# Optimization experiments

Hardware: AMD Instinct MI355X
Metric: run time of the kernel (lower is better)

The kernel has to match this reference:

```python
import jax, jax.numpy as jnp
import numpy as np

N = 100000   # points
L = 4        # SAM mask features per point (MHA kv length)
D = 256      # embed dim (out_pt_fea_dim == MHA embed_dim)
H = 4        # heads
GY = 200     # voxel grid extent used for xy_ind
C = 16       # fea_compre

def _bn(x, g, b, m, v):
    # eval-mode BatchNorm1d
    return (x - m) * jax.lax.rsqrt(v + 1e-5) * g + b

def setup_inputs():
    key = jax.random.key(0)
    ks = jax.random.split(key, 48)
    f32 = jnp.float32
    rn = lambda i, sh, s=0.05: jax.random.normal(ks[i], sh, dtype=f32) * s
    ru = lambda i, sh: jax.random.uniform(ks[i], sh, dtype=f32) + 0.5
    inp = {}
    inp['pt_fea'] = jax.random.normal(ks[0], (N, 3), dtype=f32)
    inp['xy_ind'] = jax.random.randint(ks[1], (N, 2), 0, GY, dtype=jnp.int32)
    inp['segfea'] = jax.random.normal(ks[2], (N, L, D), dtype=f32)
    inp['pixfea'] = jax.random.normal(ks[3], (N, D), dtype=f32)
    # PPmodel params (weights stored [in,out])
    dims = [3, 64, 128, 256]
    for j, d in enumerate(dims):
        inp[f'bn{j}_g'] = ru(4 + j, (d,))
        inp[f'bn{j}_b'] = rn(8 + j, (d,))
        inp[f'bn{j}_m'] = rn(12 + j, (d,))
        inp[f'bn{j}_v'] = ru(16 + j, (d,))
    inp['W1'], inp['b1'] = rn(20, (3, 64), 0.3), rn(21, (64,))
    inp['W2'], inp['b2'] = rn(22, (64, 128), 0.1), rn(23, (128,))
    inp['W3'], inp['b3'] = rn(24, (128, 256), 0.08), rn(25, (256,))
    inp['W4'], inp['b4'] = rn(26, (256, D), 0.06), rn(27, (D,))
    # MultiheadAttention params
    inp['Wq'], inp['bq'] = rn(28, (D, D)), rn(29, (D,))
    inp['Wk'], inp['bk'] = rn(30, (D, D)), rn(31, (D,))
    inp['Wv'], inp['bv'] = rn(32, (D, D)), rn(33, (D,))
    inp['Wo'], inp['bo'] = rn(34, (D, D)), rn(35, (D,))
    # to_128 and fea_compression
    inp['W128'], inp['b128'] = rn(36, (D, 128), 0.06), rn(37, (128,))
    inp['Wc'], inp['bc'] = rn(38, (128, C), 0.1), rn(39, (C,))
    return inp

def reference(pt_fea, xy_ind, segfea, pixfea,
              bn0_g, bn0_b, bn0_m, bn0_v, W1, b1,
              bn1_g, bn1_b, bn1_m, bn1_v, W2, b2,
              bn2_g, bn2_b, bn2_m, bn2_v, W3, b3,
              bn3_g, bn3_b, bn3_m, bn3_v, W4, b4,
              Wq, bq, Wk, bk, Wv, bv, Wo, bo,
              W128, b128, Wc, bc):
    # PPmodel: BN -> (Lin,BN,ReLU) x3 -> Lin
    x = _bn(pt_fea, bn0_g, bn0_b, bn0_m, bn0_v)
    x = jax.nn.relu(_bn(x @ W1 + b1, bn1_g, bn1_b, bn1_m, bn1_v))
    x = jax.nn.relu(_bn(x @ W2 + b2, bn2_g, bn2_b, bn2_m, bn2_v))
    x = jax.nn.relu(_bn(x @ W3 + b3, bn3_g, bn3_b, bn3_m, bn3_v))
    mlp = x @ W4 + b4                                   # [N, D]
    # MultiheadAttention (batch_first, query len 1, eval -> no dropout)
    dh = D // H
    q = (mlp @ Wq + bq).reshape(N, H, dh)               # [N,H,dh]
    k = (segfea @ Wk + bk).reshape(N, L, H, dh)
    v = (segfea @ Wv + bv).reshape(N, L, H, dh)
    scores = jnp.einsum('nhd,nlhd->nhl', q, k) / jnp.sqrt(jnp.float32(dh))
    attn = jax.nn.softmax(scores, axis=-1)              # [N,H,L]
    sam = jnp.einsum('nhl,nlhd->nhd', attn, v).reshape(N, D) @ Wo + bo  # [N,D]
    # unique voxel ids (single batch element -> pad index 0)
    keys = xy_ind[:, 0].astype(jnp.int32) * GY + xy_ind[:, 1].astype(jnp.int32)
    unq_keys, unq_inv, unq_cnt = jnp.unique(
        keys, return_inverse=True, return_counts=True, size=N, fill_value=GY * GY)
    valid = (unq_cnt > 0)[:, None]
    pool = lambda d: jnp.where(valid, jax.ops.segment_max(d, unq_inv, num_segments=N), 0.0)
    ori = pool(mlp) @ W128 + b128                       # scatter_max -> to_128
    seg_pooled = pool(sam)
    pix_pooled = pool(pixfea)
    processed = jax.nn.relu(ori @ Wc + bc)              # fea_compression
    unq = jnp.stack([jnp.zeros_like(unq_keys), unq_keys // GY, unq_keys % GY], axis=1).astype(jnp.int64)
    return (unq, processed, seg_pooled, pix_pooled, unq_inv)
```

## Files before the change

kernel.cpp:

```cpp
#include <hip/hip_runtime.h>
#include <math.h>
#include <stdint.h>

#define NPTS 100000
#define LKV 4
#define GYV 200
#define NBINS 40000

typedef __attribute__((ext_vector_type(8))) short bf16x8;
typedef __attribute__((ext_vector_type(8))) unsigned short u16x8;
typedef __attribute__((ext_vector_type(4))) float f32x4;

__device__ __forceinline__ unsigned short bfr(float f) {
    unsigned u = __float_as_uint(f);
    unsigned r = (u + 0x7fffu + ((u >> 16) & 1u)) >> 16;
    return (unsigned short)r;
}
__device__ __forceinline__ float fbf(unsigned short h) {
    return __uint_as_float(((unsigned)h) << 16);
}

__device__ __forceinline__ unsigned fenc(float f) {
    unsigned u = __float_as_uint(f);
    return (u & 0x80000000u) ? ~u : (u | 0x80000000u);
}
__device__ __forceinline__ float fdec(unsigned u) {
    unsigned b = (u & 0x80000000u) ? (u & 0x7fffffffu) : ~u;
    return __uint_as_float(b);
}

__global__ void kZ(unsigned* __restrict__ seg_u, unsigned* __restrict__ pix_u,
                   int* __restrict__ count)
{
    size_t idx = (size_t)blockIdx.x * 256 + threadIdx.x;
    const size_t SEG = (size_t)NPTS * 256;
    if (idx < SEG)            seg_u[idx] = 0u;
    else if (idx < 2 * SEG)   pix_u[idx - SEG] = 0u;
    else if (idx < 2 * SEG + NBINS) count[idx - 2 * SEG] = 0;
}

__global__ void kH(const int* __restrict__ xy, int* __restrict__ keys,
                   int* __restrict__ count)
{
    int i = blockIdx.x * 256 + threadIdx.x;
    if (i < NPTS) {
        int key = xy[i * 2] * GYV + xy[i * 2 + 1];
        keys[i] = key;
        atomicAdd(count + key, 1);
    }
}

__global__ __launch_bounds__(1024) void kScan(
    const int* __restrict__ count, int* __restrict__ rank,
    int* __restrict__ unqk, int* __restrict__ total)
{
    __shared__ int swcnt[16];
    __shared__ int carry_s;
    const int t = threadIdx.x, lane = t & 63, wid = t >> 6;
    if (t == 0) carry_s = 0;
    for (int chunk = 0; chunk < 40; ++chunk) {
        __syncthreads();
        int idx = chunk * 1024 + t;
        int pres = (idx < NBINS && count[idx] > 0) ? 1 : 0;
        unsigned long long mask = __ballot(pres);
        int lanepre = __popcll(mask & ((1ull << lane) - 1ull));
        if (lane == 0) swcnt[wid] = __popcll(mask);
        __syncthreads();
        if (t == 0) {
            int s = carry_s;
            for (int w = 0; w < 16; ++w) { int cn = swcnt[w]; swcnt[w] = s; s += cn; }
            carry_s = s;
        }
        __syncthreads();
        if (pres) { int e = swcnt[wid] + lanepre; rank[idx] = e; unqk[e] = idx; }
    }
    __syncthreads();
    if (t == 0) total[0] = carry_s;
}

__global__ void kU(const int* __restrict__ unqk, const int* __restrict__ total,
                   float* __restrict__ out_unq)
{
    int j = blockIdx.x * 256 + threadIdx.x;
    if (j < NPTS) {
        int k = (j < total[0]) ? unqk[j] : NBINS;
        out_unq[j * 3 + 0] = 0.f;
        out_unq[j * 3 + 1] = (float)(k / GYV);
        out_unq[j * 3 + 2] = (float)(k % GYV);
    }
}

__global__ void kConvW(const float* __restrict__ W, unsigned short* __restrict__ dst,
                       int KD, int OD)
{
    int gid = blockIdx.x * 256 + threadIdx.x;
    if (gid >= KD * OD) return;
    int k = gid / OD, n = gid - k * OD;
    int idx = ((((k >> 5) * (OD >> 4) + (n >> 4)) * 4 + ((k >> 3) & 3)) * 16 + (n & 15)) * 8 + (k & 7);
    dst[idx] = bfr(W[gid]);
}

__global__ void kConvW2(const float* __restrict__ W, unsigned short* __restrict__ dh,
                        unsigned short* __restrict__ dl, int KD, int OD)
{
    int gid = blockIdx.x * 256 + threadIdx.x;
    if (gid >= KD * OD) return;
    int k = gid / OD, n = gid - k * OD;
    int idx = ((((k >> 5) * (OD >> 4) + (n >> 4)) * 4 + ((k >> 3) & 3)) * 16 + (n & 15)) * 8 + (k & 7);
    float x = W[gid];
    unsigned short h = bfr(x);
    dh[idx] = h;
    dl[idx] = bfr(x - fbf(h));
}

template <int KD, int NTILES_TOT, int NT>
__device__ __forceinline__ void mfma_acc(
    const unsigned short* __restrict__ inbuf, const unsigned short* __restrict__ wf,
    int w, int quad, int c16, f32x4 (&acc)[4][NT])
{
    constexpr int KT = KD / 32;
    const f32x4 zz = {0.f, 0.f, 0.f, 0.f};
#pragma unroll
    for (int mt = 0; mt < 4; ++mt)
#pragma unroll
        for (int nt = 0; nt < NT; ++nt) acc[mt][nt] = zz;
#pragma unroll
    for (int kt = 0; kt < KT; ++kt) {
        bf16x8 a[4], b[NT];
        const unsigned short* ap = inbuf + ((kt * 64 + c16) * 4 + quad) * 8;
#pragma unroll
        for (int mt = 0; mt < 4; ++mt) a[mt] = *reinterpret_cast<const bf16x8*>(ap + mt * 512);
#pragma unroll
        for (int nt = 0; nt < NT; ++nt) {
            const unsigned short* bp = wf +
                (size_t)(((kt * NTILES_TOT + w * NT + nt) * 4 + quad) * 16 + c16) * 8;
            b[nt] = *reinterpret_cast<const bf16x8*>(bp);
        }
#pragma unroll
        for (int mt = 0; mt < 4; ++mt)
#pragma unroll
            for (int nt = 0; nt < NT; ++nt)
                acc[mt][nt] = __builtin_amdgcn_mfma_f32_16x16x32_bf16(a[mt], b[nt], acc[mt][nt], 0, 0, 0);
    }
}

template <int NT>
__device__ __forceinline__ void epi_bn(
    f32x4 (&acc)[4][NT], const float* lb, const float* g, const float* bb,
    const float* m, const float* v, unsigned short* __restrict__ outbuf,
    int w, int quad, int c16)
{
#pragma unroll
    for (int nt = 0; nt < NT; ++nt) {
        int n = (w * NT + nt) * 16 + c16;
        float sc = g[n] * rsqrtf(v[n] + 1e-5f);
        float mb = m[n], bbv = bb[n], lbv = lb[n];
        int nbase = ((n >> 5) * 64) * 32 + ((n >> 3) & 3) * 8 + (n & 7);
#pragma unroll
        for (int mt = 0; mt < 4; ++mt)
#pragma unroll
            for (int r = 0; r < 4; ++r) {
                int row = mt * 16 + quad * 4 + r;
                float y = fmaxf((acc[mt][nt][r] + lbv - mb) * sc + bbv, 0.f);
                outbuf[nbase + row * 32] = bfr(y);
            }
    }
}

__global__ __launch_bounds__(256) void kA(
    const float* __restrict__ pt_fea,
    const int* __restrict__ keys, const int* __restrict__ rank,
    const float* g0, const float* b0, const float* m0, const float* v0,
    const float* W1, const float* b1, const float* g1, const float* bb1, const float* m1, const float* v1,
    const unsigned short* __restrict__ w2f, const float* b2, const float* g2, const float* bb2, const float* m2, const float* v2,
    const unsigned short* __restrict__ w3f, const float* b3, const float* g3, const float* bb3, const float* m3, const float* v3,
    const unsigned short* __restrict__ w4f, const float* b4,
    const unsigned short* __restrict__ wqf, const float* bq,
    unsigned short* __restrict__ q_out, unsigned* __restrict__ seg_u)
{
    __shared__ __attribute__((aligned(16))) unsigned short bufX[64 * 256];
    __shared__ __attribute__((aligned(16))) unsigned short bufY[64 * 256];
    __shared__ float ptl[64 * 3];
    __shared__ int invs[64];
    const int t = threadIdx.x, w = t >> 6, lane = t & 63;
    const int quad = lane >> 4, c16 = lane & 15;
    const int base = blockIdx.x * 64;

    if (t < 192) {
        int p = t / 3, c = t - p * 3;
        int gp = base + p; if (gp >= NPTS) gp = NPTS - 1;
        float x = pt_fea[gp * 3 + c];
        float s = g0[c] * rsqrtf(v0[c] + 1e-5f);
        ptl[t] = (x - m0[c]) * s + b0[c];
    }
    if (t < 64 && base + t < NPTS) invs[t] = rank[keys[base + t]];
    __syncthreads();

    {
        int p = t >> 2, o0 = (t & 3) * 16;
        float x0 = ptl[p * 3], x1 = ptl[p * 3 + 1], x2 = ptl[p * 3 + 2];
#pragma unroll
        for (int j = 0; j < 16; ++j) {
            int o = o0 + j;
            float y = x0 * W1[o] + x1 * W1[64 + o] + x2 * W1[128 + o] + b1[o];
            float s = g1[o] * rsqrtf(v1[o] + 1e-5f);
            y = fmaxf((y - m1[o]) * s + bb1[o], 0.f);
            int idx = ((o >> 5) * 64 + p) * 32 + ((o >> 3) & 3) * 8 + (o & 7);
            bufX[idx] = bfr(y);
        }
    }
    __syncthreads();

    {
        f32x4 acc[4][2];
        mfma_acc<64, 8, 2>(bufX, w2f, w, quad, c16, acc);
        epi_bn<2>(acc, b2, g2, bb2, m2, v2, bufY, w, quad, c16);
    }
    __syncthreads();

    {
        f32x4 acc[4][4];
        mfma_acc<128, 16, 4>(bufY, w3f, w, quad, c16, acc);
        epi_bn<4>(acc, b3, g3, bb3, m3, v3, bufX, w, quad, c16);
    }
    __syncthreads();

    {
        f32x4 acc[4][4];
        mfma_acc<256, 16, 4>(bufX, w4f, w, quad, c16, acc);
#pragma unroll
        for (int nt = 0; nt < 4; ++nt) {
            int n = (w * 4 + nt) * 16 + c16;
            float lbv = b4[n];
            int nbase = ((n >> 5) * 64) * 32 + ((n >> 3) & 3) * 8 + (n & 7);
#pragma unroll
            for (int mt = 0; mt < 4; ++mt)
#pragma unroll
                for (int r = 0; r < 4; ++r) {
                    int row = mt * 16 + quad * 4 + r;
                    float y = acc[mt][nt][r] + lbv;
                    bufY[nbase + row * 32] = bfr(y);
                    if (base + row < NPTS)
                        atomicMax(seg_u + (size_t)invs[row] * 256 + n, fenc(y));
                }
        }
    }
    __syncthreads();

    {
        f32x4 acc[4][4];
        mfma_acc<256, 16, 4>(bufY, wqf, w, quad, c16, acc);
#pragma unroll
        for (int nt = 0; nt < 4; ++nt) {
            int n = (w * 4 + nt) * 16 + c16;
            float lbv = bq[n];
#pragma unroll
            for (int mt = 0; mt < 4; ++mt)
#pragma unroll
                for (int r = 0; r < 4; ++r) {
                    int row = mt * 16 + quad * 4 + r;
                    if (base + row < NPTS)
                        q_out[(size_t)(base + row) * 256 + n] = bfr(acc[mt][nt][r] + lbv);
                }
        }
    }
}

__global__ __launch_bounds__(256) void kC1(
    unsigned* __restrict__ seg_u, const int* __restrict__ total,
    const unsigned short* __restrict__ w128h, const unsigned short* __restrict__ w128l,
    const float* __restrict__ b128,
    const float* __restrict__ Wc, const float* __restrict__ bc,
    float* __restrict__ out_proc)
{
    __shared__ __attribute__((aligned(16))) unsigned short sb[2 * 64 * 256];
    const int t = threadIdx.x, w = t >> 6, lane = t & 63;
    const int quad = lane >> 4, c16 = lane & 15;
    const int j0 = blockIdx.x * 64;
    const int tot = total[0];

    if (j0 >= tot) {
        const int c = t & 15, r0 = (t >> 4) * 4;
        float a = bc[c];
#pragma unroll 8
        for (int k = 0; k < 128; ++k) a += b128[k] * Wc[k * 16 + c];
        a = fmaxf(a, 0.f);
#pragma unroll
        for (int rr = 0; rr < 4; ++rr) {
            int j = j0 + r0 + rr;
            if (j < NPTS) out_proc[(size_t)j * 16 + c] = a;
        }
        return;
    }

    unsigned short* fragH = sb;
    unsigned short* fragL = sb + 64 * 256;

#pragma unroll
    for (int it = 0; it < 8; ++it) {
        int ch = it * 256 + t;
        int r = ch >> 5, k0 = (ch & 31) * 8;
        int j = j0 + r;
        float x[8];
        if (j < tot) {
            unsigned* src = seg_u + (size_t)j * 256 + k0;
            uint4 u0 = *reinterpret_cast<const uint4*>(src);
            uint4 u1 = *reinterpret_cast<const uint4*>(src + 4);
            x[0] = fdec(u0.x); x[1] = fdec(u0.y); x[2] = fdec(u0.z); x[3] = fdec(u0.w);
            x[4] = fdec(u1.x); x[5] = fdec(u1.y); x[6] = fdec(u1.z); x[7] = fdec(u1.w);
            uint4 z = {0u, 0u, 0u, 0u};
            *reinterpret_cast<uint4*>(src) = z;
            *reinterpret_cast<uint4*>(src + 4) = z;
        } else {
#pragma unroll
            for (int q = 0; q < 8; ++q) x[q] = 0.f;
        }
        u16x8 hv, lv;
#pragma unroll
        for (int q = 0; q < 8; ++q) {
            unsigned short h = bfr(x[q]);
            hv[q] = h;
            lv[q] = bfr(x[q] - fbf(h));
        }
        int idx = ((k0 >> 5) * 64 + r) * 32 + ((k0 >> 3) & 3) * 8;
        *reinterpret_cast<u16x8*>(fragH + idx) = hv;
        *reinterpret_cast<u16x8*>(fragL + idx) = lv;
    }
    __syncthreads();

    f32x4 acc[4][2];
    const f32x4 zz = {0.f, 0.f, 0.f, 0.f};
#pragma unroll
    for (int mt = 0; mt < 4; ++mt)
#pragma unroll
        for (int nt = 0; nt < 2; ++nt) acc[mt][nt] = zz;
#pragma unroll
    for (int kt = 0; kt < 8; ++kt) {
        const unsigned short* aph = fragH + ((kt * 64 + c16) * 4 + quad) * 8;
        const unsigned short* apl = fragL + ((kt * 64 + c16) * 4 + quad) * 8;
        bf16x8 ah[4], al[4];
#pragma unroll
        for (int mt = 0; mt < 4; ++mt) {
            ah[mt] = *reinterpret_cast<const bf16x8*>(aph + mt * 512);
            al[mt] = *reinterpret_cast<const bf16x8*>(apl + mt * 512);
        }
#pragma unroll
        for (int nt = 0; nt < 2; ++nt) {
            size_t boff = (size_t)(((kt * 8 + w * 2 + nt) * 4 + quad) * 16 + c16) * 8;
            bf16x8 bh = *reinterpret_cast<const bf16x8*>(w128h + boff);
            bf16x8 bl = *reinterpret_cast<const bf16x8*>(w128l + boff);
#pragma unroll
            for (int mt = 0; mt < 4; ++mt) {
                acc[mt][nt] = __builtin_amdgcn_mfma_f32_16x16x32_bf16(ah[mt], bh, acc[mt][nt], 0, 0, 0);
                acc[mt][nt] = __builtin_amdgcn_mfma_f32_16x16x32_bf16(al[mt], bh, acc[mt][nt], 0, 0, 0);
                acc[mt][nt] = __builtin_amdgcn_mfma_f32_16x16x32_bf16(ah[mt], bl, acc[mt][nt], 0, 0, 0);
            }
        }
    }
    __syncthreads();

    float* ori = reinterpret_cast<float*>(sb);
#pragma unroll
    for (int nt = 0; nt < 2; ++nt) {
        int n = (w * 2 + nt) * 16 + c16;
        float bv = b128[n];
#pragma unroll
        for (int mt = 0; mt < 4; ++mt)
#pragma unroll
            for (int r = 0; r < 4; ++r)
                ori[(mt * 16 + quad * 4 + r) * 132 + n] = acc[mt][nt][r] + bv;
    }
    __syncthreads();

    {
        const int c = t & 15, r0 = (t >> 4) * 4;
        float a0 = bc[c], a1 = a0, a2 = a0, a3 = a0;
#pragma unroll 8
        for (int k = 0; k < 128; ++k) {
            float wv = Wc[k * 16 + c];
            a0 += ori[(r0 + 0) * 132 + k] * wv;
            a1 += ori[(r0 + 1) * 132 + k] * wv;
            a2 += ori[(r0 + 2) * 132 + k] * wv;
            a3 += ori[(r0 + 3) * 132 + k] * wv;
        }
        float* dst = out_proc + (size_t)(j0 + r0) * 16 + c;
        dst[0]  = fmaxf(a0, 0.f);
        dst[16] = fmaxf(a1, 0.f);
        dst[32] = fmaxf(a2, 0.f);
        dst[48] = fmaxf(a3, 0.f);
    }
}

__global__ void kP(const float* __restrict__ pixfea,
                   const int* __restrict__ keys, const int* __restrict__ rank,
                   unsigned* __restrict__ pix_u, float* __restrict__ out_inv)
{
    size_t idx = (size_t)blockIdx.x * 256 + threadIdx.x;
    int i = (int)(idx >> 8), c = (int)(idx & 255);
    int inv = rank[keys[i]];
    atomicMax(pix_u + (size_t)inv * 256 + c, fenc(pixfea[idx]));
    if (c == 0) out_inv[i] = (float)inv;
}

__global__ __launch_bounds__(256) void kB(
    const float* __restrict__ segfea, const unsigned short* __restrict__ q_in,
    const int* __restrict__ keys, const int* __restrict__ rank,
    const unsigned short* __restrict__ wkf, const unsigned short* __restrict__ wvf,
    const unsigned short* __restrict__ wof,
    const float* __restrict__ bk, const float* __restrict__ bv,
    const float* __restrict__ bo,
    unsigned* __restrict__ seg_u)
{
    __shared__ __attribute__((aligned(16))) unsigned short x_lds[64 * 256];
    __shared__ __attribute__((aligned(16))) unsigned short av_lds[16 * 256];
    __shared__ int invs[16];
    const int t = threadIdx.x, w = t >> 6, lane = t & 63;
    const int quad = lane >> 4, c16 = lane & 15;
    const int base = blockIdx.x * 16;

    {
        const float4* gsrc = reinterpret_cast<const float4*>(segfea + (size_t)base * 4 * 256);
#pragma unroll
        for (int it = 0; it < 16; ++it) {
            int e4 = it * 256 + t;
            float4 v4 = gsrc[e4];
            int r = e4 >> 6;
            int k0 = (e4 & 63) * 4;
            int idx = (((k0 >> 5) * 64 + r) * 4 + ((k0 >> 3) & 3)) * 8 + (k0 & 7);
            ushort4 u4;
            u4.x = bfr(v4.x); u4.y = bfr(v4.y); u4.z = bfr(v4.z); u4.w = bfr(v4.w);
            *reinterpret_cast<ushort4*>(x_lds + idx) = u4;
        }
    }
    if (t < 16) invs[t] = rank[keys[base + t]];
    __syncthreads();

    f32x4 acc[4][4];
    const f32x4 zz = {0.f, 0.f, 0.f, 0.f};

    mfma_acc<256, 16, 4>(x_lds, wkf, w, quad, c16, acc);

    float bkv[4], qv[4][4];
#pragma unroll
    for (int nt = 0; nt < 4; ++nt) bkv[nt] = bk[w * 64 + nt * 16 + c16];
#pragma unroll
    for (int mt = 0; mt < 4; ++mt)
#pragma unroll
        for (int nt = 0; nt < 4; ++nt)
            qv[mt][nt] = fbf(q_in[(size_t)(base + mt * 4 + quad) * 256 + w * 64 + nt * 16 + c16]);

    float sc[4][4];
#pragma unroll
    for (int mt = 0; mt < 4; ++mt) {
#pragma unroll
        for (int r = 0; r < 4; ++r) sc[mt][r] = 0.f;
#pragma unroll
        for (int nt = 0; nt < 4; ++nt)
#pragma unroll
            for (int r = 0; r < 4; ++r)
                sc[mt][r] += (acc[mt][nt][r] + bkv[nt]) * qv[mt][nt];
    }
#pragma unroll
    for (int off = 1; off < 16; off <<= 1)
#pragma unroll
        for (int mt = 0; mt < 4; ++mt)
#pragma unroll
            for (int r = 0; r < 4; ++r) sc[mt][r] += __shfl_xor(sc[mt][r], off);

    float aw[4][4];
#pragma unroll
    for (int mt = 0; mt < 4; ++mt) {
        float mx = -INFINITY;
#pragma unroll
        for (int r = 0; r < 4; ++r) { sc[mt][r] *= 0.125f; mx = fmaxf(mx, sc[mt][r]); }
        float s = 0.f;
#pragma unroll
        for (int r = 0; r < 4; ++r) { float e = __expf(sc[mt][r] - mx); aw[mt][r] = e; s += e; }
        float inv = 1.f / s;
#pragma unroll
        for (int r = 0; r < 4; ++r) aw[mt][r] *= inv;
    }

    mfma_acc<256, 16, 4>(x_lds, wvf, w, quad, c16, acc);

    float bvv[4];
#pragma unroll
    for (int nt = 0; nt < 4; ++nt) bvv[nt] = bv[w * 64 + nt * 16 + c16];
#pragma unroll
    for (int mt = 0; mt < 4; ++mt) {
#pragma unroll
        for (int nt = 0; nt < 4; ++nt) {
            float o = bvv[nt];
#pragma unroll
            for (int r = 0; r < 4; ++r) o += aw[mt][r] * acc[mt][nt][r];
            int p = mt * 4 + quad;
            int d = w * 64 + nt * 16 + c16;
            int idx = (((d >> 5) * 16 + p) * 4 + ((d >> 3) & 3)) * 8 + (d & 7);
            av_lds[idx] = bfr(o);
        }
    }
    __syncthreads();

    f32x4 acc3[4];
#pragma unroll
    for (int nt = 0; nt < 4; ++nt) acc3[nt] = zz;
#pragma unroll
    for (int kt = 0; kt < 8; ++kt) {
        bf16x8 a = *reinterpret_cast<const bf16x8*>(av_lds + ((kt * 16 + c16) * 4 + quad) * 8);
        const unsigned short* bp = wof + (size_t)(((kt * 16 + w * 4) * 4 + quad) * 16 + c16) * 8;
#pragma unroll
        for (int nt = 0; nt < 4; ++nt) {
            bf16x8 b = *reinterpret_cast<const bf16x8*>(bp + nt * 512);
            acc3[nt] = __builtin_amdgcn_mfma_f32_16x16x32_bf16(a, b, acc3[nt], 0, 0, 0);
        }
    }
#pragma unroll
    for (int nt = 0; nt < 4; ++nt) {
        float bov = bo[w * 64 + nt * 16 + c16];
#pragma unroll
        for (int r = 0; r < 4; ++r) {
            int p = quad * 4 + r;
            float sam = acc3[nt][r] + bov;
            atomicMax(seg_u + (size_t)invs[p] * 256 + w * 64 + nt * 16 + c16, fenc(sam));
        }
    }
}

__global__ void kC2(unsigned* __restrict__ seg_u, unsigned* __restrict__ pix_u,
                    const int* __restrict__ total)
{
    size_t idx = (size_t)blockIdx.x * 256 + threadIdx.x;
    const size_t SEG = (size_t)NPTS * 256;
    int tot = total[0];
    unsigned* buf = (idx < SEG) ? seg_u : pix_u;
    size_t k = (idx < SEG) ? idx : (idx - SEG);
    int j = (int)(k >> 8);
    if (j < tot) buf[k] = __float_as_uint(fdec(buf[k]));
}

extern "C" void kernel_launch(void* const* d_in, const int* in_sizes, int n_in,
                              void* d_out, int out_size, void* d_ws, size_t ws_size,
                              hipStream_t stream)
{
    const float* pt_fea = (const float*)d_in[0];
    const int*   xy     = (const int*)d_in[1];
    const float* segfea = (const float*)d_in[2];
    const float* pixfea = (const float*)d_in[3];
    const float* g0 = (const float*)d_in[4],  *b0 = (const float*)d_in[5];
    const float* m0 = (const float*)d_in[6],  *v0 = (const float*)d_in[7];
    const float* g1 = (const float*)d_in[8],  *bb1 = (const float*)d_in[9];
    const float* m1 = (const float*)d_in[10], *v1 = (const float*)d_in[11];
    const float* g2 = (const float*)d_in[12], *bb2 = (const float*)d_in[13];
    const float* m2 = (const float*)d_in[14], *v2 = (const float*)d_in[15];
    const float* g3 = (const float*)d_in[16], *bb3 = (const float*)d_in[17];
    const float* m3 = (const float*)d_in[18], *v3 = (const float*)d_in[19];
    const float* W1 = (const float*)d_in[20], *b1 = (const float*)d_in[21];
    const float* W2 = (const float*)d_in[22], *b2 = (const float*)d_in[23];
    const float* W3 = (const float*)d_in[24], *b3 = (const float*)d_in[25];
    const float* W4 = (const float*)d_in[26], *b4 = (const float*)d_in[27];
    const float* Wq = (const float*)d_in[28], *bq = (const float*)d_in[29];
    const float* Wk = (const float*)d_in[30], *bk = (const float*)d_in[31];
    const float* Wv = (const float*)d_in[32], *bv = (const float*)d_in[33];
    const float* Wo = (const float*)d_in[34], *bo = (const float*)d_in[35];
    const float* W128 = (const float*)d_in[36], *b128 = (const float*)d_in[37];
    const float* Wc = (const float*)d_in[38], *bc = (const float*)d_in[39];

    float* out = (float*)d_out;
    float* out_unq  = out;
    float* out_proc = out + (size_t)NPTS * 3;
    unsigned* seg_u = (unsigned*)(out + (size_t)NPTS * 19);
    unsigned* pix_u = (unsigned*)(out + (size_t)NPTS * 275);
    float* out_inv  = out + (size_t)NPTS * 531;

    char* ws = (char*)d_ws;
    unsigned short* wf = (unsigned short*)ws;
    unsigned short* wkf = wf;
    unsigned short* wvf = wf + 65536;
    unsigned short* wof = wf + 131072;
    unsigned short* wqf = wf + 196608;
    unsigned short* w4f = wf + 262144;
    unsigned short* w3f = wf + 327680;
    unsigned short* w2f = wf + 360448;
    unsigned short* q_bf = wf + 368640;
    int* keys  = (int*)(ws + (size_t)368640 * 2 + (size_t)NPTS * 256 * 2);
    int* rank  = keys + NPTS;
    int* count = rank + NBINS;
    int* unqk  = count + NBINS;
    int* total = unqk + NPTS;
    uintptr_t p128 = ((uintptr_t)(total + 1) + 255u) & ~(uintptr_t)255u;
    unsigned short* w128h = (unsigned short*)p128;
    unsigned short* w128l = w128h + 32768;

    const int NB16 = NPTS / 16;
    const int NB64 = (NPTS + 63) / 64;
    const size_t ZTOT = 2 * (size_t)NPTS * 256 + NBINS;
    kZ<<<(int)((ZTOT + 255) / 256), 256, 0, stream>>>(seg_u, pix_u, count);
    kH<<<(NPTS + 255) / 256, 256, 0, stream>>>(xy, keys, count);
    kScan<<<1, 1024, 0, stream>>>(count, rank, unqk, total);
    kU<<<(NPTS + 255) / 256, 256, 0, stream>>>(unqk, total, out_unq);
    kConvW<<<256, 256, 0, stream>>>(Wk, wkf, 256, 256);
    kConvW<<<256, 256, 0, stream>>>(Wv, wvf, 256, 256);
    kConvW<<<256, 256, 0, stream>>>(Wo, wof, 256, 256);
    kConvW<<<256, 256, 0, stream>>>(Wq, wqf, 256, 256);
    kConvW<<<256, 256, 0, stream>>>(W4, w4f, 256, 256);
    kConvW<<<128, 256, 0, stream>>>(W3, w3f, 128, 256);
    kConvW<<<32, 256, 0, stream>>>(W2, w2f, 64, 128);
    kConvW2<<<128, 256, 0, stream>>>(W128, w128h, w128l, 256, 128);
    kA<<<NB64, 256, 0, stream>>>(pt_fea, keys, rank,
        g0, b0, m0, v0,
        W1, b1, g1, bb1, m1, v1,
        w2f, b2, g2, bb2, m2, v2,
        w3f, b3, g3, bb3, m3, v3,
        w4f, b4, wqf, bq, q_bf, seg_u);
    kC1<<<NB64, 256, 0, stream>>>(seg_u, total, w128h, w128l, b128, Wc, bc, out_proc);
    kP<<<NPTS, 256, 0, stream>>>(pixfea, keys, rank, pix_u, out_inv);
    kB<<<NB16, 256, 0, stream>>>(segfea, q_bf, keys, rank,
        wkf, wvf, wof, bk, bv, bo, seg_u);
    kC2<<<2 * NPTS, 256, 0, stream>>>(seg_u, pix_u, total);
}
```

Measured before the change: 1.325 ms.

## Shrink LDS in kA/kB, vectorize zero and decode kernels, prefetch q

kA halves bufY and reuses bufX for the W4 output, with an extra barrier before overwriting. kB aliases av_lds onto x_lds and hoists the q loads and inverse-index lookup ahead of the segfea staging. Both kernels gain launch_bounds occupancy hints. kZ and kC2 switch to uint4 vectorized accesses, cutting thread count fourfold. The aim is more resident blocks per CU and fewer memory transactions, at the cost of extra barriers and possible register pressure from the min-blocks hint.

```diff
diff --git a/kernel.cpp b/kernel.cpp
--- a/kernel.cpp
+++ b/kernel.cpp
@@ -29,14 +29,15 @@
     return __uint_as_float(b);
 }
 
-__global__ void kZ(unsigned* __restrict__ seg_u, unsigned* __restrict__ pix_u,
-                   int* __restrict__ count)
+__global__ void kZ(uint4* __restrict__ seg_u4, uint4* __restrict__ pix_u4,
+                   uint4* __restrict__ count4)
 {
     size_t idx = (size_t)blockIdx.x * 256 + threadIdx.x;
-    const size_t SEG = (size_t)NPTS * 256;
-    if (idx < SEG)            seg_u[idx] = 0u;
-    else if (idx < 2 * SEG)   pix_u[idx - SEG] = 0u;
-    else if (idx < 2 * SEG + NBINS) count[idx - 2 * SEG] = 0;
+    const size_t SEG4 = (size_t)NPTS * 64;
+    const uint4 z = {0u, 0u, 0u, 0u};
+    if (idx < SEG4)            seg_u4[idx] = z;
+    else if (idx < 2 * SEG4)   pix_u4[idx - SEG4] = z;
+    else if (idx < 2 * SEG4 + NBINS / 4) count4[idx - 2 * SEG4] = z;
 }
 
 __global__ void kH(const int* __restrict__ xy, int* __restrict__ keys,
@@ -167,7 +168,7 @@
     }
 }
 
-__global__ __launch_bounds__(256) void kA(
+__global__ __launch_bounds__(256, 4) void kA(
     const float* __restrict__ pt_fea,
     const int* __restrict__ keys, const int* __restrict__ rank,
     const float* g0, const float* b0, const float* m0, const float* v0,
@@ -179,7 +180,7 @@
     unsigned short* __restrict__ q_out, unsigned* __restrict__ seg_u)
 {
     __shared__ __attribute__((aligned(16))) unsigned short bufX[64 * 256];
-    __shared__ __attribute__((aligned(16))) unsigned short bufY[64 * 256];
+    __shared__ __attribute__((aligned(16))) unsigned short bufY[64 * 128];
     __shared__ float ptl[64 * 3];
     __shared__ int invs[64];
     const int t = threadIdx.x, w = t >> 6, lane = t & 63;
@@ -228,6 +229,7 @@
     {
         f32x4 acc[4][4];
         mfma_acc<256, 16, 4>(bufX, w4f, w, quad, c16, acc);
+        __syncthreads();
 #pragma unroll
         for (int nt = 0; nt < 4; ++nt) {
             int n = (w * 4 + nt) * 16 + c16;
@@ -239,7 +241,7 @@
                 for (int r = 0; r < 4; ++r) {
                     int row = mt * 16 + quad * 4 + r;
                     float y = acc[mt][nt][r] + lbv;
-                    bufY[nbase + row * 32] = bfr(y);
+                    bufX[nbase + row * 32] = bfr(y);
                     if (base + row < NPTS)
                         atomicMax(seg_u + (size_t)invs[row] * 256 + n, fenc(y));
                 }
@@ -249,7 +251,7 @@
 
     {
         f32x4 acc[4][4];
-        mfma_acc<256, 16, 4>(bufY, wqf, w, quad, c16, acc);
+        mfma_acc<256, 16, 4>(bufX, wqf, w, quad, c16, acc);
 #pragma unroll
         for (int nt = 0; nt < 4; ++nt) {
             int n = (w * 4 + nt) * 16 + c16;
@@ -402,7 +404,7 @@
     if (c == 0) out_inv[i] = (float)inv;
 }
 
-__global__ __launch_bounds__(256) void kB(
+__global__ __launch_bounds__(256, 4) void kB(
     const float* __restrict__ segfea, const unsigned short* __restrict__ q_in,
     const int* __restrict__ keys, const int* __restrict__ rank,
     const unsigned short* __restrict__ wkf, const unsigned short* __restrict__ wvf,
@@ -412,11 +414,19 @@
     unsigned* __restrict__ seg_u)
 {
     __shared__ __attribute__((aligned(16))) unsigned short x_lds[64 * 256];
-    __shared__ __attribute__((aligned(16))) unsigned short av_lds[16 * 256];
     __shared__ int invs[16];
+    unsigned short* av_lds = x_lds;
     const int t = threadIdx.x, w = t >> 6, lane = t & 63;
     const int quad = lane >> 4, c16 = lane & 15;
     const int base = blockIdx.x * 16;
+
+    float qv[4][4];
+#pragma unroll
+    for (int mt = 0; mt < 4; ++mt)
+#pragma unroll
+        for (int nt = 0; nt < 4; ++nt)
+            qv[mt][nt] = fbf(q_in[(size_t)(base + mt * 4 + quad) * 256 + w * 64 + nt * 16 + c16]);
+    if (t < 16) invs[t] = rank[keys[base + t]];
 
     {
         const float4* gsrc = reinterpret_cast<const float4*>(segfea + (size_t)base * 4 * 256);
@@ -432,7 +442,6 @@
             *reinterpret_cast<ushort4*>(x_lds + idx) = u4;
         }
     }
-    if (t < 16) invs[t] = rank[keys[base + t]];
     __syncthreads();
 
     f32x4 acc[4][4];
@@ -440,14 +449,9 @@
 
     mfma_acc<256, 16, 4>(x_lds, wkf, w, quad, c16, acc);
 
-    float bkv[4], qv[4][4];
+    float bkv[4];
 #pragma unroll
     for (int nt = 0; nt < 4; ++nt) bkv[nt] = bk[w * 64 + nt * 16 + c16];
-#pragma unroll
-    for (int mt = 0; mt < 4; ++mt)
-#pragma unroll
-        for (int nt = 0; nt < 4; ++nt)
-            qv[mt][nt] = fbf(q_in[(size_t)(base + mt * 4 + quad) * 256 + w * 64 + nt * 16 + c16]);
 
     float sc[4][4];
 #pragma unroll
@@ -482,6 +486,7 @@
     }
 
     mfma_acc<256, 16, 4>(x_lds, wvf, w, quad, c16, acc);
+    __syncthreads();
 
     float bvv[4];
 #pragma unroll
@@ -526,16 +531,23 @@
     }
 }
 
-__global__ void kC2(unsigned* __restrict__ seg_u, unsigned* __restrict__ pix_u,
+__global__ void kC2(uint4* __restrict__ seg_u4, uint4* __restrict__ pix_u4,
                     const int* __restrict__ total)
 {
     size_t idx = (size_t)blockIdx.x * 256 + threadIdx.x;
-    const size_t SEG = (size_t)NPTS * 256;
+    const size_t SEG4 = (size_t)NPTS * 64;
     int tot = total[0];
-    unsigned* buf = (idx < SEG) ? seg_u : pix_u;
-    size_t k = (idx < SEG) ? idx : (idx - SEG);
-    int j = (int)(k >> 8);
-    if (j < tot) buf[k] = __float_as_uint(fdec(buf[k]));
+    uint4* buf = (idx < SEG4) ? seg_u4 : pix_u4;
+    size_t k = (idx < SEG4) ? idx : (idx - SEG4);
+    int j = (int)(k >> 6);
+    if (j < tot) {
+        uint4 u = buf[k];
+        u.x = __float_as_uint(fdec(u.x));
+        u.y = __float_as_uint(fdec(u.y));
+        u.z = __float_as_uint(fdec(u.z));
+        u.w = __float_as_uint(fdec(u.w));
+        buf[k] = u;
+    }
 }
 
 extern "C" void kernel_launch(void* const* d_in, const int* in_sizes, int n_in,
@@ -593,8 +605,8 @@
 
     const int NB16 = NPTS / 16;
     const int NB64 = (NPTS + 63) / 64;
-    const size_t ZTOT = 2 * (size_t)NPTS * 256 + NBINS;
-    kZ<<<(int)((ZTOT + 255) / 256), 256, 0, stream>>>(seg_u, pix_u, count);
+    const size_t Z4 = 2 * (size_t)NPTS * 64 + NBINS / 4;
+    kZ<<<(int)((Z4 + 255) / 256), 256, 0, stream>>>((uint4*)seg_u, (uint4*)pix_u, (uint4*)count);
     kH<<<(NPTS + 255) / 256, 256, 0, stream>>>(xy, keys, count);
     kScan<<<1, 1024, 0, stream>>>(count, rank, unqk, total);
     kU<<<(NPTS + 255) / 256, 256, 0, stream>>>(unqk, total, out_unq);
@@ -616,5 +628,5 @@
     kP<<<NPTS, 256, 0, stream>>>(pixfea, keys, rank, pix_u, out_inv);
     kB<<<NB16, 256, 0, stream>>>(segfea, q_bf, keys, rank,
         wkf, wvf, wof, bk, bv, bo, seg_u);
-    kC2<<<2 * NPTS, 256, 0, stream>>>(seg_u, pix_u, total);
-}
+    kC2<<<(int)((2 * (size_t)NPTS * 64 + 255) / 256), 256, 0, stream>>>((uint4*)seg_u, (uint4*)pix_u, total);
+}
```

Measured after the change: 2.117 ms. 59.8% more time.
